# Kernel tuning notes

Hardware: AMD Instinct MI355X
Metric: run time of the kernel (lower is better)

The kernel has to match this reference:

```python
import jax, jax.numpy as jnp
import numpy as np

TEMP = 0.1

def _normalized_grid(B, H, W, dtype=jnp.float32):
    # normalized coords in [-1, 1], (x, y) order, shape [B, H, W, 2]
    ys = jnp.linspace(-1.0, 1.0, H, dtype=dtype)
    xs = jnp.linspace(-1.0, 1.0, W, dtype=dtype)
    gy, gx = jnp.meshgrid(ys, xs, indexing='ij')
    grid = jnp.stack([gx, gy], axis=-1)  # [H, W, 2]
    return jnp.broadcast_to(grid, (B, H, W, 2))


def setup_inputs() -> dict:
    key = jax.random.key(0)
    k1, k2, k3 = jax.random.split(key, 3)
    B, H, W, D = 8, 48, 48, 1024
    f_mv_A = jax.random.normal(k1, (B, H, W, D), dtype=jnp.float32)
    f_mv_B = jax.random.normal(k2, (B, H, W, D), dtype=jnp.float32)
    # omega buffer: 2*pi*randn(dim//2, 2)
    omega = 2.0 * jnp.pi * jax.random.normal(k3, (D // 2, 2), dtype=jnp.float32)
    scale = jnp.ones((), dtype=jnp.float32)
    return {"f_mv_A": f_mv_A, "f_mv_B": f_mv_B, "omega": omega, "scale": scale}


def reference(f_mv_A, f_mv_B, omega, scale):
    B, H_A, W_A, D = f_mv_A.shape
    _, H_B, W_B, _ = f_mv_B.shape
    # Fourier positional embedding grid over image B coordinates
    x = _normalized_grid(B, H_B, W_B).reshape(B, H_B * W_B, 2)
    x_emb = x @ (scale * omega).T                      # [B, HW_B, D//2]
    pos_emb_grid = jnp.concatenate([jnp.sin(x_emb), jnp.cos(x_emb)], axis=-1)  # [B, HW_B, D]

    # cosine similarity cross-attention
    fa = f_mv_A / jnp.linalg.norm(f_mv_A, axis=-1, keepdims=True)
    fb = f_mv_B / jnp.linalg.norm(f_mv_B, axis=-1, keepdims=True)
    fa = fa.reshape(B, H_A * W_A, D)
    fb = fb.reshape(B, H_B * W_B, D)
    attn_logits = (1.0 / TEMP) * jnp.einsum('bqd,bkd->bqk', fa, fb)  # [B, HW_A, HW_B]
    attn = jax.nn.softmax(attn_logits, axis=2)
    match_emb = jnp.einsum('bqk,bkd->bqd', attn, pos_emb_grid)        # [B, HW_A, D]

    attn_logits = attn_logits.reshape(B, H_A, W_A, H_B, W_B)
    attn = attn.reshape(B, H_A, W_A, H_B, W_B)
    match_emb = match_emb.reshape(B, H_A, W_A, D)
    return attn_logits, attn, match_emb
```

## Files before the change

kernel.cpp:

```cpp
#include <hip/hip_runtime.h>
#include <stdint.h>
#include <math.h>

#define NBATCH 8
#define HWSZ   2304
#define DDIM   1024
#define NROWS  (NBATCH*HWSZ)
#define PLANE  ((size_t)NROWS*DDIM)
#define OFF1   ((size_t)NBATCH*HWSZ*HWSZ)
#define OFF2   (2*OFF1)

typedef __attribute__((ext_vector_type(8))) short bf16x8;
typedef __attribute__((ext_vector_type(8))) _Float16 f16x8;
typedef __attribute__((ext_vector_type(4))) float f32x4;

#define GLOAD16(g, l) __builtin_amdgcn_global_load_lds( \
    (const __attribute__((address_space(1))) void*)(g), \
    (__attribute__((address_space(3))) void*)(l), 16, 0, 0)

__device__ __forceinline__ float bf2f(uint16_t u) {
    union { uint32_t i; float f; } v; v.i = ((uint32_t)u) << 16; return v.f;
}
__device__ __forceinline__ uint16_t f2bf(float f) {
    union { uint32_t i; float f; } v; v.f = f;
    uint32_t x = v.i;
    return (uint16_t)((x + 0x7fffu + ((x >> 16) & 1u)) >> 16);
}
__device__ __forceinline__ float h2f(uint16_t u) {
    _Float16 h; __builtin_memcpy(&h, &u, 2); return (float)h;
}
__device__ __forceinline__ uint16_t f2h(float f) {
    _Float16 h = (_Float16)f; uint16_t u; __builtin_memcpy(&u, &h, 2); return u;
}
__device__ __forceinline__ int dmode(const uint16_t* s) {
    uint16_t v = s[0];
    return (v == 0x3F80u) ? 1 : ((v == 0x3C00u) ? 2 : 0);
}
__device__ __forceinline__ float dec16(uint16_t u, int m) { return (m == 1) ? bf2f(u) : h2f(u); }
__device__ __forceinline__ uint16_t enc16(float f, int m) { return (m == 1) ? f2bf(f) : f2h(f); }

__global__ void layout_probe(int* __restrict__ rowT, int* __restrict__ colT) {
    int lane = threadIdx.x & 63;
    int m = lane & 15, q = lane >> 4;
    bf16x8 a1, b1, a2, b2;
    #pragma unroll
    for (int j = 0; j < 8; j++) {
        int k = q * 8 + j;
        float k0 = (k == 0) ? 1.0f : 0.0f;
        a1[j] = (short)f2bf(k0);
        b1[j] = (short)f2bf(k0 * (float)(m + 1));
        a2[j] = (short)f2bf(k0 * (float)(m + 1));
        b2[j] = (short)f2bf(k0);
    }
    f32x4 z = {0.f, 0.f, 0.f, 0.f};
    f32x4 d1 = __builtin_amdgcn_mfma_f32_16x16x32_bf16(a1, b1, z, 0, 0, 0);
    f32x4 d2 = __builtin_amdgcn_mfma_f32_16x16x32_bf16(a2, b2, z, 0, 0, 0);
    #pragma unroll
    for (int r = 0; r < 4; r++) {
        colT[lane * 4 + r] = (int)d1[r] - 1;
        rowT[lane * 4 + r] = (int)d2[r] - 1;
    }
}

__global__ void rownorm_kernel(const void* __restrict__ inA, const void* __restrict__ inB,
                               const uint16_t* __restrict__ scalep, float* __restrict__ rn,
                               void* __restrict__ outbase) {
    const int mode = dmode(scalep);
    int row = blockIdx.x;
    int t = threadIdx.x;
    const void* src = (row < NROWS) ? inA : inB;
    int lrow = (row < NROWS) ? row : row - NROWS;
    float v[4];
    if (mode == 0) {
        const float* p = (const float*)src + (size_t)lrow * DDIM + t * 4;
        float4 f = *(const float4*)p;
        v[0] = f.x; v[1] = f.y; v[2] = f.z; v[3] = f.w;
        uint16_t* hbase = (uint16_t*)((float*)outbase + OFF1) + ((row < NROWS) ? 0 : PLANE);
        uint16_t h0 = f2h(v[0]), h1 = f2h(v[1]), h2 = f2h(v[2]), h3 = f2h(v[3]);
        uint2 hv;
        hv.x = (uint32_t)h0 | ((uint32_t)h1 << 16);
        hv.y = (uint32_t)h2 | ((uint32_t)h3 << 16);
        *(uint2*)(hbase + (size_t)lrow * DDIM + t * 4) = hv;
    } else {
        const uint16_t* p = (const uint16_t*)src + (size_t)lrow * DDIM + t * 4;
        uint2 u = *(const uint2*)p;
        v[0] = dec16(u.x & 0xffff, mode); v[1] = dec16(u.x >> 16, mode);
        v[2] = dec16(u.y & 0xffff, mode); v[3] = dec16(u.y >> 16, mode);
    }
    float ss = v[0]*v[0] + v[1]*v[1] + v[2]*v[2] + v[3]*v[3];
    __shared__ float red[256];
    red[t] = ss; __syncthreads();
    for (int s = 128; s > 0; s >>= 1) { if (t < s) red[t] += red[t + s]; __syncthreads(); }
    if (t == 0) rn[row] = 1.0f / sqrtf(red[0]);
}

__global__ void posemb_kernel(const void* __restrict__ omega, const uint16_t* __restrict__ scalep,
                              uint16_t* __restrict__ posT) {
    const int mode = dmode(scalep);
    int j = blockIdx.x;
    float om0, om1, sc;
    if (mode == 0) {
        const float* om = (const float*)omega;
        om0 = om[j * 2]; om1 = om[j * 2 + 1];
        sc = *(const float*)scalep;
    } else {
        const uint16_t* om = (const uint16_t*)omega;
        om0 = dec16(om[j * 2], mode); om1 = dec16(om[j * 2 + 1], mode);
        sc = dec16(scalep[0], mode);
    }
    om0 *= sc; om1 *= sc;
    for (int p = threadIdx.x; p < HWSZ; p += 256) {
        int iy = p / 48, ix = p % 48;
        float gx = (2.0f / 47.0f) * (float)ix - 1.0f;
        float gy = (2.0f / 47.0f) * (float)iy - 1.0f;
        float e = om0 * gx + om1 * gy;
        size_t chunk = (size_t)(p >> 5) * (DDIM * 32);
        int kin = p & 31;
        posT[chunk + (size_t)j * 32 + kin]           = f2bf(sinf(e));
        posT[chunk + (size_t)(j + 512) * 32 + kin]   = f2bf(cosf(e));
    }
}

__launch_bounds__(256, 2)
__global__ void gemm1_mfma(const void* __restrict__ inA, const void* __restrict__ inB,
                           const uint16_t* __restrict__ scalep, const float* __restrict__ rn,
                           void* __restrict__ outbase,
                           const int* __restrict__ rowT, const int* __restrict__ colT) {
    const int mode = dmode(scalep);
    __shared__ uint16_t sA[128 * 32];
    __shared__ uint16_t sB[128 * 32];
    __shared__ float rnS[256];
    int g = blockIdx.x;
    int swz = (g & 7) * 324 + (g >> 3);
    int b = swz / 324;
    int rr = swz % 324;
    int tm = rr / 18, tn = rr % 18;
    int t = threadIdx.x;
    if (t < 128) rnS[t] = 10.0f * rn[(size_t)b * HWSZ + tm * 128 + t];
    else         rnS[t] = rn[(size_t)NROWS + (size_t)b * HWSZ + tn * 128 + (t - 128)];
    int lane = t & 63, wave = t >> 6;
    int wm = (wave & 1) * 64, wn = (wave >> 1) * 64;
    int lr = lane & 15, ko = (lane >> 4) * 8;
    size_t rowA0 = (size_t)b * HWSZ + tm * 128;
    size_t rowB0 = (size_t)b * HWSZ + tn * 128;
    const uint16_t* pA16;
    const uint16_t* pB16;
    if (mode == 0) {
        const uint16_t* planes = (const uint16_t*)((const float*)outbase + OFF1);
        pA16 = planes + rowA0 * DDIM;
        pB16 = planes + PLANE + rowB0 * DDIM;
    } else {
        pA16 = (const uint16_t*)inA + rowA0 * DDIM;
        pB16 = (const uint16_t*)inB + rowB0 * DDIM;
    }
    int srow = wave * 32 + (lane >> 2);
    int squart = (lane & 3) * 8;
    const uint16_t* aS0 = pA16 + (size_t)srow * DDIM + squart;
    const uint16_t* aS1 = aS0 + (size_t)16 * DDIM;
    const uint16_t* bS0 = pB16 + (size_t)srow * DDIM + squart;
    const uint16_t* bS1 = bS0 + (size_t)16 * DDIM;
    uint16_t* aD0 = sA + (wave * 32) * 32;
    uint16_t* aD1 = aD0 + 512;
    uint16_t* bD0 = sB + (wave * 32) * 32;
    uint16_t* bD1 = bD0 + 512;
    f32x4 acc[4][4] = {};

    for (int k0 = 0; k0 < DDIM; k0 += 32) {
        __syncthreads();
        GLOAD16(aS0 + k0, aD0);
        GLOAD16(aS1 + k0, aD1);
        GLOAD16(bS0 + k0, bD0);
        GLOAD16(bS1 + k0, bD1);
        __syncthreads();
        if (mode == 1) {
            bf16x8 af[4], bf_[4];
            #pragma unroll
            for (int i = 0; i < 4; i++) af[i] = *(const bf16x8*)(sA + (wm + i * 16 + lr) * 32 + ko);
            #pragma unroll
            for (int j = 0; j < 4; j++) bf_[j] = *(const bf16x8*)(sB + (wn + j * 16 + lr) * 32 + ko);
            #pragma unroll
            for (int i = 0; i < 4; i++)
                #pragma unroll
                for (int j = 0; j < 4; j++)
                    acc[i][j] = __builtin_amdgcn_mfma_f32_16x16x32_bf16(af[i], bf_[j], acc[i][j], 0, 0, 0);
        } else {
            f16x8 af[4], bf_[4];
            #pragma unroll
            for (int i = 0; i < 4; i++) af[i] = *(const f16x8*)(sA + (wm + i * 16 + lr) * 32 + ko);
            #pragma unroll
            for (int j = 0; j < 4; j++) bf_[j] = *(const f16x8*)(sB + (wn + j * 16 + lr) * 32 + ko);
            #pragma unroll
            for (int i = 0; i < 4; i++)
                #pragma unroll
                for (int j = 0; j < 4; j++)
                    acc[i][j] = __builtin_amdgcn_mfma_f32_16x16x32_f16(af[i], bf_[j], acc[i][j], 0, 0, 0);
        }
    }

    int rtab[4], ctab[4];
    #pragma unroll
    for (int r = 0; r < 4; r++) {
        rtab[r] = rowT[lane * 4 + r] & 15;
        ctab[r] = colT[lane * 4 + r] & 15;
    }
    size_t cbase = (size_t)b * HWSZ * HWSZ;
    #pragma unroll
    for (int i = 0; i < 4; i++) {
        #pragma unroll
        for (int j = 0; j < 4; j++) {
            #pragma unroll
            for (int r = 0; r < 4; r++) {
                int row = wm + i * 16 + rtab[r];
                int col = wn + j * 16 + ctab[r];
                float v = acc[i][j][r] * rnS[row] * rnS[128 + col];
                size_t gm = (size_t)(tm * 128 + row);
                size_t gn = (size_t)(tn * 128 + col);
                if (mode == 0) ((float*)outbase)[cbase + gm * HWSZ + gn] = v;
                else ((uint16_t*)outbase)[cbase + gm * HWSZ + gn] = enc16(v, mode);
            }
        }
    }
}

__global__ void softmax_p16(void* __restrict__ outbase, const uint16_t* __restrict__ scalep,
                            uint16_t* __restrict__ p16) {
    const int mode = dmode(scalep);
    size_t row = blockIdx.x;
    int t = threadIdx.x;
    float v[9];
    if (mode == 0) {
        const float* src = (const float*)outbase + row * HWSZ;
        #pragma unroll
        for (int i = 0; i < 9; i++) v[i] = src[i * 256 + t];
    } else {
        const uint16_t* src = (const uint16_t*)outbase + row * HWSZ;
        #pragma unroll
        for (int i = 0; i < 9; i++) v[i] = dec16(src[i * 256 + t], mode);
    }
    float m = v[0];
    #pragma unroll
    for (int i = 1; i < 9; i++) m = fmaxf(m, v[i]);
    __shared__ float red[256];
    red[t] = m; __syncthreads();
    for (int s = 128; s > 0; s >>= 1) { if (t < s) red[t] = fmaxf(red[t], red[t + s]); __syncthreads(); }
    float M = red[0];
    __syncthreads();
    float ssum = 0.0f;
    #pragma unroll
    for (int i = 0; i < 9; i++) { v[i] = __expf(v[i] - M); ssum += v[i]; }
    red[t] = ssum; __syncthreads();
    for (int s = 128; s > 0; s >>= 1) { if (t < s) red[t] += red[t + s]; __syncthreads(); }
    float inv = 1.0f / red[0];
    uint16_t* prow = p16 + row * HWSZ;
    if (mode == 0) {
        float* dst = (float*)outbase + OFF1 + row * HWSZ;
        #pragma unroll
        for (int i = 0; i < 9; i++) {
            float p = v[i] * inv;
            dst[i * 256 + t] = p;
            prow[i * 256 + t] = f2bf(p);
        }
    } else {
        uint16_t* dst = (uint16_t*)outbase + OFF1 + row * HWSZ;
        #pragma unroll
        for (int i = 0; i < 9; i++) {
            uint16_t pk = enc16(v[i] * inv, mode);
            dst[i * 256 + t] = pk;
            prow[i * 256 + t] = (mode == 1) ? pk : f2bf(h2f(pk));
        }
    }
}

__global__ void rowstat_kernel(const void* __restrict__ outbase, const uint16_t* __restrict__ scalep,
                               float* __restrict__ stats) {
    const int mode = dmode(scalep);
    size_t row = blockIdx.x;
    int t = threadIdx.x;
    float v[9];
    if (mode == 0) {
        const float* src = (const float*)outbase + row * HWSZ;
        #pragma unroll
        for (int i = 0; i < 9; i++) v[i] = src[i * 256 + t];
    } else {
        const uint16_t* src = (const uint16_t*)outbase + row * HWSZ;
        #pragma unroll
        for (int i = 0; i < 9; i++) v[i] = dec16(src[i * 256 + t], mode);
    }
    float m = v[0];
    #pragma unroll
    for (int i = 1; i < 9; i++) m = fmaxf(m, v[i]);
    __shared__ float red[256];
    red[t] = m; __syncthreads();
    for (int s = 128; s > 0; s >>= 1) { if (t < s) red[t] = fmaxf(red[t], red[t + s]); __syncthreads(); }
    float M = red[0];
    __syncthreads();
    float ssum = 0.0f;
    #pragma unroll
    for (int i = 0; i < 9; i++) ssum += __expf(v[i] - M);
    red[t] = ssum; __syncthreads();
    for (int s = 128; s > 0; s >>= 1) { if (t < s) red[t] += red[t + s]; __syncthreads(); }
    if (t == 0) { stats[row] = M; stats[NROWS + row] = 1.0f / red[0]; }
}

#define G2BM 64
#define G2BN 256
#define G2L  40

__launch_bounds__(256, 4)
__global__ void gemm2_p16(void* __restrict__ outbase, const uint16_t* __restrict__ posT,
                          const uint16_t* __restrict__ scalep, const uint16_t* __restrict__ p16,
                          const int* __restrict__ rowT, const int* __restrict__ colT) {
    const int mode = dmode(scalep);
    __shared__ uint16_t sA[G2BM * 32];
    __shared__ uint16_t sB[G2BN * 32];
    int g = blockIdx.x;
    int swz = (g & 7) * 144 + (g >> 3);
    int b = swz / 144;
    int rr = swz % 144;
    int tm = rr >> 2, tn = rr & 3;
    int t = threadIdx.x;
    int lane = t & 63, wave = t >> 6;
    int wn = wave * 64;
    int lr = lane & 15, ko = (lane >> 4) * 8;
    const uint16_t* aS = p16 + ((size_t)b * HWSZ + (size_t)tm * G2BM + wave * 16 + (lane >> 2)) * HWSZ
                             + (lane & 3) * 8;
    uint16_t* aD = sA + (wave * 16) * 32;
    uint16_t* bD = sB + (wave * 64) * 32;
    f32x4 acc[4][4] = {};
    for (int k0 = 0; k0 < HWSZ; k0 += 32) {
        const uint16_t* bS = posT + (size_t)(k0 >> 5) * (DDIM * 32)
                                  + ((size_t)tn * G2BN + wave * 64) * 32 + lane * 8;
        __syncthreads();
        GLOAD16(aS + k0, aD);
        GLOAD16(bS + 0 * 512, bD + 0 * 512);
        GLOAD16(bS + 1 * 512, bD + 1 * 512);
        GLOAD16(bS + 2 * 512, bD + 2 * 512);
        GLOAD16(bS + 3 * 512, bD + 3 * 512);
        __syncthreads();
        bf16x8 af[4], bfr[4];
        #pragma unroll
        for (int i = 0; i < 4; i++) af[i] = *(const bf16x8*)(sA + (i * 16 + lr) * 32 + ko);
        #pragma unroll
        for (int j = 0; j < 4; j++) bfr[j] = *(const bf16x8*)(sB + (wn + j * 16 + lr) * 32 + ko);
        #pragma unroll
        for (int i = 0; i < 4; i++)
            #pragma unroll
            for (int j = 0; j < 4; j++)
                acc[i][j] = __builtin_amdgcn_mfma_f32_16x16x32_bf16(af[i], bfr[j], acc[i][j], 0, 0, 0);
    }
    int rtab[4], ctab[4];
    #pragma unroll
    for (int r = 0; r < 4; r++) {
        rtab[r] = rowT[lane * 4 + r] & 15;
        ctab[r] = colT[lane * 4 + r] & 15;
    }
    #pragma unroll
    for (int i = 0; i < 4; i++) {
        #pragma unroll
        for (int j = 0; j < 4; j++) {
            #pragma unroll
            for (int r = 0; r < 4; r++) {
                size_t row = (size_t)tm * G2BM + i * 16 + rtab[r];
                size_t col = (size_t)tn * G2BN + wn + j * 16 + ctab[r];
                size_t idx = OFF2 + (size_t)b * HWSZ * DDIM + row * DDIM + col;
                if (mode == 0) ((float*)outbase)[idx] = acc[i][j][r];
                else ((uint16_t*)outbase)[idx] = enc16(acc[i][j][r], mode);
            }
        }
    }
}

__launch_bounds__(256, 4)
__global__ void gemm2_mfma(void* __restrict__ outbase, const uint16_t* __restrict__ posT,
                           const uint16_t* __restrict__ scalep, const float* __restrict__ stats,
                           const int* __restrict__ rowT, const int* __restrict__ colT) {
    const int mode = dmode(scalep);
    __shared__ uint16_t sA[G2BM * G2L];
    int g = blockIdx.x;
    int swz = (g & 7) * 144 + (g >> 3);
    int b = swz / 144;
    int rr = swz % 144;
    int tm = rr >> 2, tn = rr & 3;
    int t = threadIdx.x;
    int lane = t & 63, wave = t >> 6;
    int wn = wave * 64;
    int lr = lane & 15, ko = (lane >> 4) * 8;
    int ar = t >> 2, ac8 = (t & 3) * 8;
    size_t grow = (size_t)b * HWSZ + (size_t)tm * G2BM + ar;
    float Mrow = stats[grow];
    float invl = stats[NROWS + grow];
    f32x4 acc[4][4] = {};
    for (int k0 = 0; k0 < HWSZ; k0 += 32) {
        uint16_t av[8];
        float p[8];
        if (mode == 0) {
            const float* ap = (const float*)outbase + grow * HWSZ + k0 + ac8;
            float4 x0 = *(const float4*)ap, x1 = *(const float4*)(ap + 4);
            p[0] = __expf(x0.x - Mrow) * invl; p[1] = __expf(x0.y - Mrow) * invl;
            p[2] = __expf(x0.z - Mrow) * invl; p[3] = __expf(x0.w - Mrow) * invl;
            p[4] = __expf(x1.x - Mrow) * invl; p[5] = __expf(x1.y - Mrow) * invl;
            p[6] = __expf(x1.z - Mrow) * invl; p[7] = __expf(x1.w - Mrow) * invl;
            if (tn == 0) {
                float* dst = (float*)outbase + OFF1 + grow * HWSZ + k0 + ac8;
                *(float4*)dst       = *(const float4*)p;
                *(float4*)(dst + 4) = *(const float4*)(p + 4);
            }
        } else {
            const uint16_t* ap = (const uint16_t*)outbase + grow * HWSZ + k0 + ac8;
            uint4 r0 = *(const uint4*)ap;
            const uint16_t* u0 = (const uint16_t*)&r0;
            #pragma unroll
            for (int j = 0; j < 8; j++) p[j] = __expf(dec16(u0[j], mode) - Mrow) * invl;
            if (tn == 0) {
                uint16_t pk[8];
                #pragma unroll
                for (int j = 0; j < 8; j++) pk[j] = enc16(p[j], mode);
                *(uint4*)((uint16_t*)outbase + OFF1 + grow * HWSZ + k0 + ac8) = *(const uint4*)pk;
            }
        }
        #pragma unroll
        for (int j = 0; j < 8; j++) av[j] = f2bf(p[j]);
        __syncthreads();
        *(uint4*)(sA + ar * G2L + ac8) = *(const uint4*)av;
        __syncthreads();
        const uint16_t* bchunk = posT + (size_t)(k0 >> 5) * (DDIM * 32);
        bf16x8 af[4], bfr[4];
        #pragma unroll
        for (int j = 0; j < 4; j++)
            bfr[j] = *(const bf16x8*)(bchunk + ((size_t)tn * G2BN + wn + j * 16 + lr) * 32 + ko);
        #pragma unroll
        for (int i = 0; i < 4; i++) af[i] = *(const bf16x8*)(sA + (i * 16 + lr) * G2L + ko);
        #pragma unroll
        for (int i = 0; i < 4; i++)
            #pragma unroll
            for (int j = 0; j < 4; j++)
                acc[i][j] = __builtin_amdgcn_mfma_f32_16x16x32_bf16(af[i], bfr[j], acc[i][j], 0, 0, 0);
    }
    int rtab[4], ctab[4];
    #pragma unroll
    for (int r = 0; r < 4; r++) {
        rtab[r] = rowT[lane * 4 + r] & 15;
        ctab[r] = colT[lane * 4 + r] & 15;
    }
    #pragma unroll
    for (int i = 0; i < 4; i++) {
        #pragma unroll
        for (int j = 0; j < 4; j++) {
            #pragma unroll
            for (int r = 0; r < 4; r++) {
                size_t row = (size_t)tm * G2BM + i * 16 + rtab[r];
                size_t col = (size_t)tn * G2BN + wn + j * 16 + ctab[r];
                size_t idx = OFF2 + (size_t)b * HWSZ * DDIM + row * DDIM + col;
                if (mode == 0) ((float*)outbase)[idx] = acc[i][j][r];
                else ((uint16_t*)outbase)[idx] = enc16(acc[i][j][r], mode);
            }
        }
    }
}

extern "C" void kernel_launch(void* const* d_in, const int* in_sizes, int n_in,
                              void* d_out, int out_size, void* d_ws, size_t ws_size,
                              hipStream_t stream) {
    const void* fA    = d_in[0];
    const void* fB    = d_in[1];
    const void* omega = d_in[2];
    const uint16_t* scale = (const uint16_t*)d_in[3];

    int* rowT = (int*)d_ws;
    int* colT = rowT + 256;
    float* rn = (float*)((char*)d_ws + 4096);
    size_t posT_off = 4096 + (size_t)2 * NROWS * 4;
    uint16_t* posT = (uint16_t*)((char*)d_ws + posT_off);
    size_t p16_off = posT_off + (size_t)DDIM * HWSZ * 2;
    size_t ws_need = p16_off + (size_t)NROWS * HWSZ * 2;
    uint16_t* p16 = (uint16_t*)((char*)d_ws + p16_off);
    const bool big_ws = (ws_size >= ws_need);

    layout_probe<<<1, 64, 0, stream>>>(rowT, colT);
    rownorm_kernel<<<2 * NROWS, 256, 0, stream>>>(fA, fB, scale, rn, d_out);
    posemb_kernel<<<512, 256, 0, stream>>>(omega, scale, posT);

    gemm1_mfma<<<18 * 18 * NBATCH, 256, 0, stream>>>(fA, fB, scale, rn, d_out, rowT, colT);

    if (big_ws) {
        softmax_p16<<<NROWS, 256, 0, stream>>>(d_out, scale, p16);
        gemm2_p16<<<(HWSZ / G2BM) * (DDIM / G2BN) * NBATCH, 256, 0, stream>>>(
            d_out, posT, scale, p16, rowT, colT);
    } else {
        rowstat_kernel<<<NROWS, 256, 0, stream>>>(d_out, scale, rn);
        gemm2_mfma<<<(HWSZ / G2BM) * (DDIM / G2BN) * NBATCH, 256, 0, stream>>>(
            d_out, posT, scale, rn, rowT, colT);
    }
}
```

Baseline: 428.7 us.

## Merge prep kernels, deepen K tiles in both GEMMs, retile gemm2

Fuses the layout probe, positional-embedding and row-norm kernels into one prep launch so fewer kernel launches are paid. gemm1 now stages 64-wide K slices per barrier pair, which halves the number of sync rounds, and its launch bound rises to 3 blocks per SM. gemm2_p16 is retiled to 32x256 output tiles with 64-wide K steps and twice as many blocks. The larger shared-memory tiles may reduce occupancy or cause LDS bank conflicts.

```diff
diff --git a/kernel.cpp b/kernel.cpp
--- a/kernel.cpp
+++ b/kernel.cpp
@@ -39,35 +39,65 @@
 __device__ __forceinline__ float dec16(uint16_t u, int m) { return (m == 1) ? bf2f(u) : h2f(u); }
 __device__ __forceinline__ uint16_t enc16(float f, int m) { return (m == 1) ? f2bf(f) : f2h(f); }
 
-__global__ void layout_probe(int* __restrict__ rowT, int* __restrict__ colT) {
-    int lane = threadIdx.x & 63;
-    int m = lane & 15, q = lane >> 4;
-    bf16x8 a1, b1, a2, b2;
-    #pragma unroll
-    for (int j = 0; j < 8; j++) {
-        int k = q * 8 + j;
-        float k0 = (k == 0) ? 1.0f : 0.0f;
-        a1[j] = (short)f2bf(k0);
-        b1[j] = (short)f2bf(k0 * (float)(m + 1));
-        a2[j] = (short)f2bf(k0 * (float)(m + 1));
-        b2[j] = (short)f2bf(k0);
-    }
-    f32x4 z = {0.f, 0.f, 0.f, 0.f};
-    f32x4 d1 = __builtin_amdgcn_mfma_f32_16x16x32_bf16(a1, b1, z, 0, 0, 0);
-    f32x4 d2 = __builtin_amdgcn_mfma_f32_16x16x32_bf16(a2, b2, z, 0, 0, 0);
-    #pragma unroll
-    for (int r = 0; r < 4; r++) {
-        colT[lane * 4 + r] = (int)d1[r] - 1;
-        rowT[lane * 4 + r] = (int)d2[r] - 1;
-    }
-}
-
-__global__ void rownorm_kernel(const void* __restrict__ inA, const void* __restrict__ inB,
-                               const uint16_t* __restrict__ scalep, float* __restrict__ rn,
-                               void* __restrict__ outbase) {
+__global__ void prep_kernel(const void* __restrict__ inA, const void* __restrict__ inB,
+                            const void* __restrict__ omega, const uint16_t* __restrict__ scalep,
+                            float* __restrict__ rn, uint16_t* __restrict__ posT,
+                            int* __restrict__ rowT, int* __restrict__ colT,
+                            void* __restrict__ outbase) {
     const int mode = dmode(scalep);
-    int row = blockIdx.x;
+    int g = blockIdx.x;
     int t = threadIdx.x;
+    if (g == 0) {
+        if (t < 64) {
+            int lane = t;
+            int m = lane & 15, q = lane >> 4;
+            bf16x8 a1, b1, a2, b2;
+            #pragma unroll
+            for (int j = 0; j < 8; j++) {
+                int k = q * 8 + j;
+                float k0 = (k == 0) ? 1.0f : 0.0f;
+                a1[j] = (short)f2bf(k0);
+                b1[j] = (short)f2bf(k0 * (float)(m + 1));
+                a2[j] = (short)f2bf(k0 * (float)(m + 1));
+                b2[j] = (short)f2bf(k0);
+            }
+            f32x4 z = {0.f, 0.f, 0.f, 0.f};
+            f32x4 d1 = __builtin_amdgcn_mfma_f32_16x16x32_bf16(a1, b1, z, 0, 0, 0);
+            f32x4 d2 = __builtin_amdgcn_mfma_f32_16x16x32_bf16(a2, b2, z, 0, 0, 0);
+            #pragma unroll
+            for (int r = 0; r < 4; r++) {
+                colT[lane * 4 + r] = (int)d1[r] - 1;
+                rowT[lane * 4 + r] = (int)d2[r] - 1;
+            }
+        }
+        return;
+    }
+    if (g <= 512) {
+        int j = g - 1;
+        float om0, om1, sc;
+        if (mode == 0) {
+            const float* om = (const float*)omega;
+            om0 = om[j * 2]; om1 = om[j * 2 + 1];
+            sc = *(const float*)scalep;
+        } else {
+            const uint16_t* om = (const uint16_t*)omega;
+            om0 = dec16(om[j * 2], mode); om1 = dec16(om[j * 2 + 1], mode);
+            sc = dec16(scalep[0], mode);
+        }
+        om0 *= sc; om1 *= sc;
+        for (int p = t; p < HWSZ; p += 256) {
+            int iy = p / 48, ix = p % 48;
+            float gx = (2.0f / 47.0f) * (float)ix - 1.0f;
+            float gy = (2.0f / 47.0f) * (float)iy - 1.0f;
+            float e = om0 * gx + om1 * gy;
+            size_t chunk = (size_t)(p >> 5) * (DDIM * 32);
+            int kin = p & 31;
+            posT[chunk + (size_t)j * 32 + kin]           = f2bf(sinf(e));
+            posT[chunk + (size_t)(j + 512) * 32 + kin]   = f2bf(cosf(e));
+        }
+        return;
+    }
+    int row = g - 513;
     const void* src = (row < NROWS) ? inA : inB;
     int lrow = (row < NROWS) ? row : row - NROWS;
     float v[4];
@@ -94,41 +124,14 @@
     if (t == 0) rn[row] = 1.0f / sqrtf(red[0]);
 }
 
-__global__ void posemb_kernel(const void* __restrict__ omega, const uint16_t* __restrict__ scalep,
-                              uint16_t* __restrict__ posT) {
-    const int mode = dmode(scalep);
-    int j = blockIdx.x;
-    float om0, om1, sc;
-    if (mode == 0) {
-        const float* om = (const float*)omega;
-        om0 = om[j * 2]; om1 = om[j * 2 + 1];
-        sc = *(const float*)scalep;
-    } else {
-        const uint16_t* om = (const uint16_t*)omega;
-        om0 = dec16(om[j * 2], mode); om1 = dec16(om[j * 2 + 1], mode);
-        sc = dec16(scalep[0], mode);
-    }
-    om0 *= sc; om1 *= sc;
-    for (int p = threadIdx.x; p < HWSZ; p += 256) {
-        int iy = p / 48, ix = p % 48;
-        float gx = (2.0f / 47.0f) * (float)ix - 1.0f;
-        float gy = (2.0f / 47.0f) * (float)iy - 1.0f;
-        float e = om0 * gx + om1 * gy;
-        size_t chunk = (size_t)(p >> 5) * (DDIM * 32);
-        int kin = p & 31;
-        posT[chunk + (size_t)j * 32 + kin]           = f2bf(sinf(e));
-        posT[chunk + (size_t)(j + 512) * 32 + kin]   = f2bf(cosf(e));
-    }
-}
-
-__launch_bounds__(256, 2)
+__launch_bounds__(256, 3)
 __global__ void gemm1_mfma(const void* __restrict__ inA, const void* __restrict__ inB,
                            const uint16_t* __restrict__ scalep, const float* __restrict__ rn,
                            void* __restrict__ outbase,
                            const int* __restrict__ rowT, const int* __restrict__ colT) {
     const int mode = dmode(scalep);
-    __shared__ uint16_t sA[128 * 32];
-    __shared__ uint16_t sB[128 * 32];
+    __shared__ uint16_t sA[128 * 64];
+    __shared__ uint16_t sB[128 * 64];
     __shared__ float rnS[256];
     int g = blockIdx.x;
     int swz = (g & 7) * 324 + (g >> 3);
@@ -153,47 +156,50 @@
         pA16 = (const uint16_t*)inA + rowA0 * DDIM;
         pB16 = (const uint16_t*)inB + rowB0 * DDIM;
     }
-    int srow = wave * 32 + (lane >> 2);
-    int squart = (lane & 3) * 8;
-    const uint16_t* aS0 = pA16 + (size_t)srow * DDIM + squart;
-    const uint16_t* aS1 = aS0 + (size_t)16 * DDIM;
-    const uint16_t* bS0 = pB16 + (size_t)srow * DDIM + squart;
-    const uint16_t* bS1 = bS0 + (size_t)16 * DDIM;
-    uint16_t* aD0 = sA + (wave * 32) * 32;
-    uint16_t* aD1 = aD0 + 512;
-    uint16_t* bD0 = sB + (wave * 32) * 32;
-    uint16_t* bD1 = bD0 + 512;
+    int srow = lane >> 3;
+    int scol = (lane & 7) * 8;
+    const uint16_t* aS = pA16 + (size_t)(wave * 32 + srow) * DDIM + scol;
+    const uint16_t* bS = pB16 + (size_t)(wave * 32 + srow) * DDIM + scol;
+    uint16_t* aD = sA + (wave * 32) * 64;
+    uint16_t* bD = sB + (wave * 32) * 64;
     f32x4 acc[4][4] = {};
 
-    for (int k0 = 0; k0 < DDIM; k0 += 32) {
+    for (int k0 = 0; k0 < DDIM; k0 += 64) {
         __syncthreads();
-        GLOAD16(aS0 + k0, aD0);
-        GLOAD16(aS1 + k0, aD1);
-        GLOAD16(bS0 + k0, bD0);
-        GLOAD16(bS1 + k0, bD1);
+        #pragma unroll
+        for (int s = 0; s < 4; s++) {
+            GLOAD16(aS + (size_t)(s * 8) * DDIM + k0, aD + (s * 8) * 64);
+            GLOAD16(bS + (size_t)(s * 8) * DDIM + k0, bD + (s * 8) * 64);
+        }
         __syncthreads();
         if (mode == 1) {
-            bf16x8 af[4], bf_[4];
-            #pragma unroll
-            for (int i = 0; i < 4; i++) af[i] = *(const bf16x8*)(sA + (wm + i * 16 + lr) * 32 + ko);
-            #pragma unroll
-            for (int j = 0; j < 4; j++) bf_[j] = *(const bf16x8*)(sB + (wn + j * 16 + lr) * 32 + ko);
-            #pragma unroll
-            for (int i = 0; i < 4; i++)
-                #pragma unroll
-                for (int j = 0; j < 4; j++)
-                    acc[i][j] = __builtin_amdgcn_mfma_f32_16x16x32_bf16(af[i], bf_[j], acc[i][j], 0, 0, 0);
+            #pragma unroll
+            for (int kk = 0; kk < 2; kk++) {
+                bf16x8 af[4], bf_[4];
+                #pragma unroll
+                for (int i = 0; i < 4; i++) af[i] = *(const bf16x8*)(sA + (wm + i * 16 + lr) * 64 + kk * 32 + ko);
+                #pragma unroll
+                for (int j = 0; j < 4; j++) bf_[j] = *(const bf16x8*)(sB + (wn + j * 16 + lr) * 64 + kk * 32 + ko);
+                #pragma unroll
+                for (int i = 0; i < 4; i++)
+                    #pragma unroll
+                    for (int j = 0; j < 4; j++)
+                        acc[i][j] = __builtin_amdgcn_mfma_f32_16x16x32_bf16(af[i], bf_[j], acc[i][j], 0, 0, 0);
+            }
         } else {
-            f16x8 af[4], bf_[4];
-            #pragma unroll
-            for (int i = 0; i < 4; i++) af[i] = *(const f16x8*)(sA + (wm + i * 16 + lr) * 32 + ko);
-            #pragma unroll
-            for (int j = 0; j < 4; j++) bf_[j] = *(const f16x8*)(sB + (wn + j * 16 + lr) * 32 + ko);
-            #pragma unroll
-            for (int i = 0; i < 4; i++)
-                #pragma unroll
-                for (int j = 0; j < 4; j++)
-                    acc[i][j] = __builtin_amdgcn_mfma_f32_16x16x32_f16(af[i], bf_[j], acc[i][j], 0, 0, 0);
+            #pragma unroll
+            for (int kk = 0; kk < 2; kk++) {
+                f16x8 af[4], bf_[4];
+                #pragma unroll
+                for (int i = 0; i < 4; i++) af[i] = *(const f16x8*)(sA + (wm + i * 16 + lr) * 64 + kk * 32 + ko);
+                #pragma unroll
+                for (int j = 0; j < 4; j++) bf_[j] = *(const f16x8*)(sB + (wn + j * 16 + lr) * 64 + kk * 32 + ko);
+                #pragma unroll
+                for (int i = 0; i < 4; i++)
+                    #pragma unroll
+                    for (int j = 0; j < 4; j++)
+                        acc[i][j] = __builtin_amdgcn_mfma_f32_16x16x32_f16(af[i], bf_[j], acc[i][j], 0, 0, 0);
+            }
         }
     }
 
@@ -311,42 +317,49 @@
                           const uint16_t* __restrict__ scalep, const uint16_t* __restrict__ p16,
                           const int* __restrict__ rowT, const int* __restrict__ colT) {
     const int mode = dmode(scalep);
-    __shared__ uint16_t sA[G2BM * 32];
-    __shared__ uint16_t sB[G2BN * 32];
+    __shared__ uint16_t sA[32 * 64];
+    __shared__ uint16_t sB[2 * 256 * 32];
     int g = blockIdx.x;
-    int swz = (g & 7) * 144 + (g >> 3);
-    int b = swz / 144;
-    int rr = swz % 144;
+    int swz = (g & 7) * 288 + (g >> 3);
+    int b = swz / 288;
+    int rr = swz % 288;
     int tm = rr >> 2, tn = rr & 3;
     int t = threadIdx.x;
     int lane = t & 63, wave = t >> 6;
     int wn = wave * 64;
     int lr = lane & 15, ko = (lane >> 4) * 8;
-    const uint16_t* aS = p16 + ((size_t)b * HWSZ + (size_t)tm * G2BM + wave * 16 + (lane >> 2)) * HWSZ
-                             + (lane & 3) * 8;
-    uint16_t* aD = sA + (wave * 16) * 32;
-    uint16_t* bD = sB + (wave * 64) * 32;
-    f32x4 acc[4][4] = {};
-    for (int k0 = 0; k0 < HWSZ; k0 += 32) {
-        const uint16_t* bS = posT + (size_t)(k0 >> 5) * (DDIM * 32)
-                                  + ((size_t)tn * G2BN + wave * 64) * 32 + lane * 8;
+    const uint16_t* aS = p16 + ((size_t)b * HWSZ + (size_t)tm * 32 + wave * 8 + (lane >> 3)) * HWSZ
+                             + (lane & 7) * 8;
+    uint16_t* aD = sA + (wave * 8) * 64;
+    int bd = lane >> 2;
+    int bq = (lane & 3) * 8;
+    f32x4 acc[2][4] = {};
+    for (int k0 = 0; k0 < HWSZ; k0 += 64) {
         __syncthreads();
         GLOAD16(aS + k0, aD);
-        GLOAD16(bS + 0 * 512, bD + 0 * 512);
-        GLOAD16(bS + 1 * 512, bD + 1 * 512);
-        GLOAD16(bS + 2 * 512, bD + 2 * 512);
-        GLOAD16(bS + 3 * 512, bD + 3 * 512);
+        #pragma unroll
+        for (int kk = 0; kk < 2; kk++) {
+            const uint16_t* bS = posT + ((size_t)(k0 >> 5) + kk) * (DDIM * 32)
+                                      + ((size_t)tn * 256 + wave * 64 + bd) * 32 + bq;
+            uint16_t* bDk = sB + kk * (256 * 32) + (wave * 64) * 32;
+            #pragma unroll
+            for (int s = 0; s < 4; s++)
+                GLOAD16(bS + (size_t)(s * 16) * 32, bDk + (s * 16) * 32);
+        }
         __syncthreads();
-        bf16x8 af[4], bfr[4];
-        #pragma unroll
-        for (int i = 0; i < 4; i++) af[i] = *(const bf16x8*)(sA + (i * 16 + lr) * 32 + ko);
-        #pragma unroll
-        for (int j = 0; j < 4; j++) bfr[j] = *(const bf16x8*)(sB + (wn + j * 16 + lr) * 32 + ko);
-        #pragma unroll
-        for (int i = 0; i < 4; i++)
-            #pragma unroll
-            for (int j = 0; j < 4; j++)
-                acc[i][j] = __builtin_amdgcn_mfma_f32_16x16x32_bf16(af[i], bfr[j], acc[i][j], 0, 0, 0);
+        #pragma unroll
+        for (int kk = 0; kk < 2; kk++) {
+            bf16x8 af[2], bfr[4];
+            #pragma unroll
+            for (int i = 0; i < 2; i++) af[i] = *(const bf16x8*)(sA + (i * 16 + lr) * 64 + kk * 32 + ko);
+            #pragma unroll
+            for (int j = 0; j < 4; j++) bfr[j] = *(const bf16x8*)(sB + kk * (256 * 32) + (wn + j * 16 + lr) * 32 + ko);
+            #pragma unroll
+            for (int i = 0; i < 2; i++)
+                #pragma unroll
+                for (int j = 0; j < 4; j++)
+                    acc[i][j] = __builtin_amdgcn_mfma_f32_16x16x32_bf16(af[i], bfr[j], acc[i][j], 0, 0, 0);
+        }
     }
     int rtab[4], ctab[4];
     #pragma unroll
@@ -355,13 +368,13 @@
         ctab[r] = colT[lane * 4 + r] & 15;
     }
     #pragma unroll
-    for (int i = 0; i < 4; i++) {
+    for (int i = 0; i < 2; i++) {
         #pragma unroll
         for (int j = 0; j < 4; j++) {
             #pragma unroll
             for (int r = 0; r < 4; r++) {
-                size_t row = (size_t)tm * G2BM + i * 16 + rtab[r];
-                size_t col = (size_t)tn * G2BN + wn + j * 16 + ctab[r];
+                size_t row = (size_t)tm * 32 + i * 16 + rtab[r];
+                size_t col = (size_t)tn * 256 + wn + j * 16 + ctab[r];
                 size_t idx = OFF2 + (size_t)b * HWSZ * DDIM + row * DDIM + col;
                 if (mode == 0) ((float*)outbase)[idx] = acc[i][j][r];
                 else ((uint16_t*)outbase)[idx] = enc16(acc[i][j][r], mode);
@@ -476,15 +489,14 @@
     uint16_t* p16 = (uint16_t*)((char*)d_ws + p16_off);
     const bool big_ws = (ws_size >= ws_need);
 
-    layout_probe<<<1, 64, 0, stream>>>(rowT, colT);
-    rownorm_kernel<<<2 * NROWS, 256, 0, stream>>>(fA, fB, scale, rn, d_out);
-    posemb_kernel<<<512, 256, 0, stream>>>(omega, scale, posT);
+    prep_kernel<<<513 + 2 * NROWS, 256, 0, stream>>>(fA, fB, omega, scale, rn, posT,
+                                                     rowT, colT, d_out);
 
     gemm1_mfma<<<18 * 18 * NBATCH, 256, 0, stream>>>(fA, fB, scale, rn, d_out, rowT, colT);
 
     if (big_ws) {
         softmax_p16<<<NROWS, 256, 0, stream>>>(d_out, scale, p16);
-        gemm2_p16<<<(HWSZ / G2BM) * (DDIM / G2BN) * NBATCH, 256, 0, stream>>>(
+        gemm2_p16<<<(HWSZ / 32) * (DDIM / 256) * NBATCH, 256, 0, stream>>>(
             d_out, posT, scale, p16, rowT, colT);
     } else {
         rowstat_kernel<<<NROWS, 256, 0, stream>>>(d_out, scale, rn);
```

New measurement: 447.6 us. 4.4% more time.
